# Optimization experiments

Hardware: AMD Instinct MI355X
Metric: run time of the kernel (lower is better)

The kernel has to match this reference:

```python
import jax, jax.numpy as jnp
import numpy as np

LN_EPS = 1e-5  # torch.nn.LayerNorm default


def setup_inputs() -> dict:
    key = jax.random.key(0)
    k1, k2 = jax.random.split(key)
    C = 64
    x = jax.random.normal(k1, (1, C, 64, 96, 96), dtype=jnp.float32)
    ln_gamma = jnp.ones((C,), jnp.float32)
    ln_beta = jnp.zeros((C,), jnp.float32)
    # Conv3d(C, 3C, 1, groups=C) -> per-channel scalar weight [3C] and bias [3C]
    conv_w = jax.random.normal(k2, (3 * C,), dtype=jnp.float32) * 0.02
    conv_b = jnp.zeros((3 * C,), jnp.float32)
    return {"x": x, "ln_gamma": ln_gamma, "ln_beta": ln_beta,
            "conv_w": conv_w, "conv_b": conv_b}


def reference(x, ln_gamma, ln_beta, conv_w, conv_b):
    B, C, D, H, W = x.shape
    N = D * H * W
    xf = x.reshape(B, C, N)  # [B, C, N]

    # LayerNorm over the channel dim (module permutes channels last)
    mean = jnp.mean(xf, axis=1, keepdims=True)
    var = jnp.mean(jnp.square(xf - mean), axis=1, keepdims=True)
    y = (xf - mean) * jax.lax.rsqrt(var + LN_EPS)
    y = y * ln_gamma[None, :, None] + ln_beta[None, :, None]

    # grouped 1x1x1 conv: output channel o reads input channel o // 3
    idx = jnp.arange(3 * C) // 3
    y3 = y[:, idx, :] * conv_w[None, :, None] + conv_b[None, :, None]  # [B, 3C, N]
    q, k, v = jnp.split(y3, 3, axis=1)  # each [B, C, N]

    # channel (cross-covariance) attention: logits [B, C, C]
    logits = jnp.einsum('bcn,bkn->bck', q, k) * (C ** -0.5)
    attn = jax.nn.softmax(logits, axis=-1)  # max-subtraction built in
    out = jnp.einsum('bck,bkn->bcn', attn, v).reshape(B, C, D, H, W)
    return x + out
```

## Files before the change

### kernel.cpp

```cpp
#include <hip/hip_runtime.h>

#define NPOS 589824
#define LN_EPS 1e-5f

typedef _Float16 half8 __attribute__((ext_vector_type(8)));
typedef float f32x4 __attribute__((ext_vector_type(4)));

#define K1_BLOCKS 768
#define CPB 3

__global__ __launch_bounds__(256) void csa_k1(
    const float* __restrict__ x, const float* __restrict__ lng,
    const float* __restrict__ lnb, float* __restrict__ partials,
    float* __restrict__ gfin, int partial_mode)
{
    __shared__ __align__(16) _Float16 Aar[32][264];
    __shared__ __align__(16) _Float16 Bar[32][264];
    const int tid = threadIdx.x;
    const int lane = tid & 63;
    const int wv = tid >> 6;

    #pragma unroll
    for (int r = 22; r < 32; ++r) {
        const _Float16 v = (r == 22) ? (_Float16)1.0f : (_Float16)0.0f;
        for (int ci = tid; ci < 264; ci += 256) { Aar[r][ci] = v; Bar[r][ci] = v; }
    }
    f32x4 acc00 = {0.f,0.f,0.f,0.f}, acc01 = acc00, acc10 = acc00, acc11 = acc00;
    const int row = lane & 15;
    const int kbase = wv * 64 + ((lane >> 4) << 3);
    const int pos0 = blockIdx.x * (CPB * 256);

    for (int ck = 0; ck < CPB; ++ck) {
        const int n = pos0 + ck * 256 + tid;
        float s = 0.f, sq = 0.f;
        float xv[43];
        #pragma unroll
        for (int c = 0; c < 43; ++c) {
            float v = x[c * NPOS + n];
            xv[c] = v; s += v; sq = fmaf(v, v, sq);
        }
        #pragma unroll
        for (int c = 43; c < 64; ++c) {
            float v = x[c * NPOS + n];
            s += v; sq = fmaf(v, v, sq);
        }
        const float mu  = s * (1.f/64.f);
        const float var = fmaf(-mu, mu, sq * (1.f/64.f));
        const float rin = rsqrtf(fmaxf(var, 0.f) + LN_EPS);
        #pragma unroll
        for (int c = 0; c < 43; ++c) {
            float yv = fmaf((xv[c] - mu) * rin, lng[c], lnb[c]);
            _Float16 h = (_Float16)yv;
            if (c < 22)  Aar[c][tid] = h;
            if (c >= 21) Bar[c - 21][tid] = h;
        }
        __syncthreads();
        #pragma unroll
        for (int s2 = 0; s2 < 2; ++s2) {
            const int kk = kbase + s2 * 32;
            half8 a0 = *(const half8*)&Aar[row][kk];
            half8 a1 = *(const half8*)&Aar[row + 16][kk];
            half8 b0 = *(const half8*)&Bar[row][kk];
            half8 b1 = *(const half8*)&Bar[row + 16][kk];
            acc00 = __builtin_amdgcn_mfma_f32_16x16x32_f16(a0, b0, acc00, 0, 0, 0);
            acc01 = __builtin_amdgcn_mfma_f32_16x16x32_f16(a0, b1, acc01, 0, 0, 0);
            acc10 = __builtin_amdgcn_mfma_f32_16x16x32_f16(a1, b0, acc10, 0, 0, 0);
            acc11 = __builtin_amdgcn_mfma_f32_16x16x32_f16(a1, b1, acc11, 0, 0, 0);
        }
        __syncthreads();
    }
    float* G32 = (float*)&Aar[0][0];
    for (int e = tid; e < 1024; e += 256) G32[e] = 0.f;
    __syncthreads();
    const int r0 = (lane >> 4) * 4, c0 = lane & 15;
    #pragma unroll
    for (int r = 0; r < 4; ++r) {
        atomicAdd(&G32[(r0 + r) * 32 + c0],            acc00[r]);
        atomicAdd(&G32[(r0 + r) * 32 + 16 + c0],       acc01[r]);
        atomicAdd(&G32[(16 + r0 + r) * 32 + c0],       acc10[r]);
        atomicAdd(&G32[(16 + r0 + r) * 32 + 16 + c0],  acc11[r]);
    }
    __syncthreads();
    if (partial_mode) {
        for (int e = tid; e < 1024; e += 256) partials[blockIdx.x * 1024 + e] = G32[e];
    } else {
        for (int e = tid; e < 1024; e += 256) atomicAdd(&gfin[e], G32[e]);
    }
}

__global__ __launch_bounds__(256) void csa_k2(const float* __restrict__ partials,
                                              float* __restrict__ gfin)
{
    const int e = blockIdx.x * 256 + threadIdx.x;
    float s = 0.f;
    for (int b = 0; b < K1_BLOCKS; ++b) s += partials[b * 1024 + e];
    gfin[e] = s;
}

__global__ void csa_k3(const float* __restrict__ G, const float* __restrict__ cw,
                       const float* __restrict__ cb, float* __restrict__ M,
                       float* __restrict__ betaO)
{
    const int c = threadIdx.x;
    __shared__ float lg[64][65];
    const float wq = cw[c], bq = cb[c];
    const int a = c / 3;
    const float Sa = G[a * 32 + 22];
    float mx = -1e30f;
    #pragma unroll
    for (int k = 0; k < 64; ++k) {
        const float wk = cw[64 + k], bk = cb[64 + k];
        const int b = (64 + k) / 3 - 21;
        const float Gab = G[a * 32 + b];
        const float Sb  = G[22 * 32 + b];
        float lo = 0.125f * (wq * wk * Gab + wq * bk * Sa + bq * wk * Sb
                             + bq * bk * (float)NPOS);
        lg[c][k] = lo;
        mx = fmaxf(mx, lo);
    }
    float sum = 0.f;
    #pragma unroll
    for (int k = 0; k < 64; ++k) {
        float e = expf(lg[c][k] - mx);
        lg[c][k] = e; sum += e;
    }
    const float inv = 1.f / sum;
    float Ml[22];
    #pragma unroll
    for (int m = 0; m < 22; ++m) Ml[m] = 0.f;
    float bacc = 0.f;
    #pragma unroll
    for (int k = 0; k < 64; ++k) {
        const float attn = lg[c][k] * inv;
        const int mm = (128 + k) / 3 - 42;
        Ml[mm] = fmaf(attn, cw[128 + k], Ml[mm]);
        bacc   = fmaf(attn, cb[128 + k], bacc);
    }
    #pragma unroll
    for (int m = 0; m < 22; ++m) M[c * 22 + m] = Ml[m];
    betaO[c] = bacc;
}

__global__ __launch_bounds__(256) void csa_k4(
    const float* __restrict__ x, const float* __restrict__ lng,
    const float* __restrict__ lnb, const float* __restrict__ M,
    const float* __restrict__ betaO, float* __restrict__ out)
{
    const int n = blockIdx.x * 256 + threadIdx.x;
    float xv[64];
    float s = 0.f, sq = 0.f;
    #pragma unroll
    for (int c = 0; c < 64; ++c) {
        float v = x[c * NPOS + n];
        xv[c] = v; s += v; sq = fmaf(v, v, sq);
    }
    const float mu  = s * (1.f/64.f);
    const float var = fmaf(-mu, mu, sq * (1.f/64.f));
    const float rin = rsqrtf(fmaxf(var, 0.f) + LN_EPS);
    float y[22];
    #pragma unroll
    for (int m = 0; m < 22; ++m)
        y[m] = fmaf((xv[42 + m] - mu) * rin, lng[42 + m], lnb[42 + m]);
    #pragma unroll
    for (int c = 0; c < 64; ++c) {
        float acc = betaO[c];
        #pragma unroll
        for (int m = 0; m < 22; ++m)
            acc = fmaf(M[c * 22 + m], y[m], acc);
        out[c * NPOS + n] = xv[c] + acc;
    }
}

extern "C" void kernel_launch(void* const* d_in, const int* in_sizes, int n_in,
                              void* d_out, int out_size, void* d_ws, size_t ws_size,
                              hipStream_t stream) {
    const float* x   = (const float*)d_in[0];
    const float* lng = (const float*)d_in[1];
    const float* lnb = (const float*)d_in[2];
    const float* cw  = (const float*)d_in[3];
    const float* cb  = (const float*)d_in[4];
    float* out = (float*)d_out;

    float* wsf = (float*)d_ws;
    float* Gf  = wsf;
    float* Mf  = wsf + 1024;
    float* Bf  = wsf + 1024 + 64 * 22;
    float* Pf  = wsf + 4096;

    const size_t need = 16384 + (size_t)K1_BLOCKS * 1024 * 4;
    const int partial = (ws_size >= need) ? 1 : 0;
    if (!partial) hipMemsetAsync(Gf, 0, 1024 * sizeof(float), stream);

    hipLaunchKernelGGL(csa_k1, dim3(K1_BLOCKS), dim3(256), 0, stream,
                       x, lng, lnb, Pf, Gf, partial);
    if (partial)
        hipLaunchKernelGGL(csa_k2, dim3(4), dim3(256), 0, stream, Pf, Gf);
    hipLaunchKernelGGL(csa_k3, dim3(1), dim3(64), 0, stream, Gf, cw, cb, Mf, Bf);
    hipLaunchKernelGGL(csa_k4, dim3(NPOS / 256), dim3(256), 0, stream,
                       x, lng, lnb, Mf, Bf, out);
}
```

Before: 172.3 us.

## Precompute LayerNorm stats in separate pass and reuse in gram and output kernels

Adds a vectorized stats kernel that computes per-position mean and inverse std once and stores them to workspace. The gram kernel then reads only the 43 channels it needs instead of all 64. The output kernel reads stats instead of recomputing them and uses nontemporal stores. This trades an extra full read of x plus a stats buffer for less work and traffic in the gram kernel, and keeps the old path as a fallback when the workspace is small.

Measured after the change: 170.7 us. Within noise of the previous version (-0.9%).

```diff
diff --git a/kernel.cpp b/kernel.cpp
--- a/kernel.cpp
+++ b/kernel.cpp
@@ -5,14 +5,40 @@
 
 typedef _Float16 half8 __attribute__((ext_vector_type(8)));
 typedef float f32x4 __attribute__((ext_vector_type(4)));
+typedef float f32x2 __attribute__((ext_vector_type(2)));
 
 #define K1_BLOCKS 768
 #define CPB 3
 
-__global__ __launch_bounds__(256) void csa_k1(
+
+__global__ __launch_bounds__(256) void csa_stats(
+    const float* __restrict__ x, float* __restrict__ stats )
+{
+    const int g = blockIdx.x * 256 + threadIdx.x;
+    const f32x4* __restrict__ x4 = (const f32x4*)x;
+    f32x4 s = {0.f,0.f,0.f,0.f}, sq = s;
+    #pragma unroll
+    for (int c = 0; c < 64; ++c) {
+        f32x4 v = x4[c * (NPOS/4) + g];
+        s += v;
+        sq += v * v;
+    }
+    f32x4 mu = s * (1.f/64.f);
+    f32x4 var = sq * (1.f/64.f) - mu * mu;
+    f32x4 rin;
+    #pragma unroll
+    for (int j = 0; j < 4; ++j) rin[j] = rsqrtf(fmaxf(var[j], 0.f) + LN_EPS);
+    f32x4* st4 = (f32x4*)stats;
+    f32x4 o0 = {mu[0], rin[0], mu[1], rin[1]};
+    f32x4 o1 = {mu[2], rin[2], mu[3], rin[3]};
+    st4[2*g]     = o0;
+    st4[2*g + 1] = o1;
+}
+
+__global__ __launch_bounds__(256) void csa_gram(
     const float* __restrict__ x, const float* __restrict__ lng,
-    const float* __restrict__ lnb, float* __restrict__ partials,
-    float* __restrict__ gfin, int partial_mode)
+    const float* __restrict__ lnb, const float* __restrict__ stats,
+    float* __restrict__ partials, float* __restrict__ gfin, int partial_mode)
 {
     __shared__ __align__(16) _Float16 Aar[32][264];
     __shared__ __align__(16) _Float16 Bar[32][264];
@@ -29,27 +55,16 @@
     const int row = lane & 15;
     const int kbase = wv * 64 + ((lane >> 4) << 3);
     const int pos0 = blockIdx.x * (CPB * 256);
+    const f32x2* __restrict__ st2 = (const f32x2*)stats;
 
     for (int ck = 0; ck < CPB; ++ck) {
         const int n = pos0 + ck * 256 + tid;
-        float s = 0.f, sq = 0.f;
-        float xv[43];
+        const f32x2 st = st2[n];
+        const float mu = st[0], rin = st[1];
         #pragma unroll
         for (int c = 0; c < 43; ++c) {
             float v = x[c * NPOS + n];
-            xv[c] = v; s += v; sq = fmaf(v, v, sq);
-        }
-        #pragma unroll
-        for (int c = 43; c < 64; ++c) {
-            float v = x[c * NPOS + n];
-            s += v; sq = fmaf(v, v, sq);
-        }
-        const float mu  = s * (1.f/64.f);
-        const float var = fmaf(-mu, mu, sq * (1.f/64.f));
-        const float rin = rsqrtf(fmaxf(var, 0.f) + LN_EPS);
-        #pragma unroll
-        for (int c = 0; c < 43; ++c) {
-            float yv = fmaf((xv[c] - mu) * rin, lng[c], lnb[c]);
+            float yv = fmaf((v - mu) * rin, lng[c], lnb[c]);
             _Float16 h = (_Float16)yv;
             if (c < 22)  Aar[c][tid] = h;
             if (c >= 21) Bar[c - 21][tid] = h;
@@ -143,6 +158,120 @@
 
 __global__ __launch_bounds__(256) void csa_k4(
     const float* __restrict__ x, const float* __restrict__ lng,
+    const float* __restrict__ lnb, const float* __restrict__ stats,
+    const float* __restrict__ M, const float* __restrict__ betaO,
+    float* __restrict__ out)
+{
+    const int n = blockIdx.x * 256 + threadIdx.x;
+    const f32x2 st = ((const f32x2*)stats)[n];
+    const float mu = st[0], rin = st[1];
+    float y[22], xr[22];
+    #pragma unroll
+    for (int m = 0; m < 22; ++m) {
+        float v = x[(42 + m) * NPOS + n];
+        xr[m] = v;
+        y[m] = fmaf((v - mu) * rin, lng[42 + m], lnb[42 + m]);
+    }
+    #pragma unroll
+    for (int c = 0; c < 42; ++c) {
+        float v = x[c * NPOS + n];
+        float acc = betaO[c];
+        #pragma unroll
+        for (int m = 0; m < 22; ++m)
+            acc = fmaf(M[c * 22 + m], y[m], acc);
+        __builtin_nontemporal_store(v + acc, &out[c * NPOS + n]);
+    }
+    #pragma unroll
+    for (int c = 42; c < 64; ++c) {
+        float acc = betaO[c];
+        #pragma unroll
+        for (int m = 0; m < 22; ++m)
+            acc = fmaf(M[c * 22 + m], y[m], acc);
+        __builtin_nontemporal_store(xr[c - 42] + acc, &out[c * NPOS + n]);
+    }
+}
+
+__global__ __launch_bounds__(256) void csa_k1f(
+    const float* __restrict__ x, const float* __restrict__ lng,
+    const float* __restrict__ lnb, float* __restrict__ partials,
+    float* __restrict__ gfin, int partial_mode)
+{
+    __shared__ __align__(16) _Float16 Aar[32][264];
+    __shared__ __align__(16) _Float16 Bar[32][264];
+    const int tid = threadIdx.x;
+    const int lane = tid & 63;
+    const int wv = tid >> 6;
+
+    #pragma unroll
+    for (int r = 22; r < 32; ++r) {
+        const _Float16 v = (r == 22) ? (_Float16)1.0f : (_Float16)0.0f;
+        for (int ci = tid; ci < 264; ci += 256) { Aar[r][ci] = v; Bar[r][ci] = v; }
+    }
+    f32x4 acc00 = {0.f,0.f,0.f,0.f}, acc01 = acc00, acc10 = acc00, acc11 = acc00;
+    const int row = lane & 15;
+    const int kbase = wv * 64 + ((lane >> 4) << 3);
+    const int pos0 = blockIdx.x * (CPB * 256);
+
+    for (int ck = 0; ck < CPB; ++ck) {
+        const int n = pos0 + ck * 256 + tid;
+        float s = 0.f, sq = 0.f;
+        float xv[43];
+        #pragma unroll
+        for (int c = 0; c < 43; ++c) {
+            float v = x[c * NPOS + n];
+            xv[c] = v; s += v; sq = fmaf(v, v, sq);
+        }
+        #pragma unroll
+        for (int c = 43; c < 64; ++c) {
+            float v = x[c * NPOS + n];
+            s += v; sq = fmaf(v, v, sq);
+        }
+        const float mu  = s * (1.f/64.f);
+        const float var = fmaf(-mu, mu, sq * (1.f/64.f));
+        const float rin = rsqrtf(fmaxf(var, 0.f) + LN_EPS);
+        #pragma unroll
+        for (int c = 0; c < 43; ++c) {
+            float yv = fmaf((xv[c] - mu) * rin, lng[c], lnb[c]);
+            _Float16 h = (_Float16)yv;
+            if (c < 22)  Aar[c][tid] = h;
+            if (c >= 21) Bar[c - 21][tid] = h;
+        }
+        __syncthreads();
+        #pragma unroll
+        for (int s2 = 0; s2 < 2; ++s2) {
+            const int kk = kbase + s2 * 32;
+            half8 a0 = *(const half8*)&Aar[row][kk];
+            half8 a1 = *(const half8*)&Aar[row + 16][kk];
+            half8 b0 = *(const half8*)&Bar[row][kk];
+            half8 b1 = *(const half8*)&Bar[row + 16][kk];
+            acc00 = __builtin_amdgcn_mfma_f32_16x16x32_f16(a0, b0, acc00, 0, 0, 0);
+            acc01 = __builtin_amdgcn_mfma_f32_16x16x32_f16(a0, b1, acc01, 0, 0, 0);
+            acc10 = __builtin_amdgcn_mfma_f32_16x16x32_f16(a1, b0, acc10, 0, 0, 0);
+            acc11 = __builtin_amdgcn_mfma_f32_16x16x32_f16(a1, b1, acc11, 0, 0, 0);
+        }
+        __syncthreads();
+    }
+    float* G32 = (float*)&Aar[0][0];
+    for (int e = tid; e < 1024; e += 256) G32[e] = 0.f;
+    __syncthreads();
+    const int r0 = (lane >> 4) * 4, c0 = lane & 15;
+    #pragma unroll
+    for (int r = 0; r < 4; ++r) {
+        atomicAdd(&G32[(r0 + r) * 32 + c0],            acc00[r]);
+        atomicAdd(&G32[(r0 + r) * 32 + 16 + c0],       acc01[r]);
+        atomicAdd(&G32[(16 + r0 + r) * 32 + c0],       acc10[r]);
+        atomicAdd(&G32[(16 + r0 + r) * 32 + 16 + c0],  acc11[r]);
+    }
+    __syncthreads();
+    if (partial_mode) {
+        for (int e = tid; e < 1024; e += 256) partials[blockIdx.x * 1024 + e] = G32[e];
+    } else {
+        for (int e = tid; e < 1024; e += 256) atomicAdd(&gfin[e], G32[e]);
+    }
+}
+
+__global__ __launch_bounds__(256) void csa_k4f(
+    const float* __restrict__ x, const float* __restrict__ lng,
     const float* __restrict__ lnb, const float* __restrict__ M,
     const float* __restrict__ betaO, float* __restrict__ out)
 {
@@ -170,6 +299,7 @@
         out[c * NPOS + n] = xv[c] + acc;
     }
 }
+
 
 extern "C" void kernel_launch(void* const* d_in, const int* in_sizes, int n_in,
                               void* d_out, int out_size, void* d_ws, size_t ws_size,
@@ -185,17 +315,33 @@
     float* Gf  = wsf;
     float* Mf  = wsf + 1024;
     float* Bf  = wsf + 1024 + 64 * 22;
-    float* Pf  = wsf + 4096;
-
-    const size_t need = 16384 + (size_t)K1_BLOCKS * 1024 * 4;
-    const int partial = (ws_size >= need) ? 1 : 0;
-    if (!partial) hipMemsetAsync(Gf, 0, 1024 * sizeof(float), stream);
-
-    hipLaunchKernelGGL(csa_k1, dim3(K1_BLOCKS), dim3(256), 0, stream,
-                       x, lng, lnb, Pf, Gf, partial);
-    if (partial)
+
+    const size_t statsOffB = 16384;
+    const size_t partOffB  = statsOffB + (size_t)NPOS * 8;
+    const size_t needFull  = partOffB + (size_t)K1_BLOCKS * 1024 * 4;
+
+    if (ws_size >= needFull) {
+        float* stats = (float*)((char*)d_ws + statsOffB);
+        float* Pf    = (float*)((char*)d_ws + partOffB);
+        hipLaunchKernelGGL(csa_stats, dim3(NPOS / 1024), dim3(256), 0, stream,
+                           x, stats);
+        hipLaunchKernelGGL(csa_gram, dim3(K1_BLOCKS), dim3(256), 0, stream,
+                           x, lng, lnb, stats, Pf, Gf, 1);
         hipLaunchKernelGGL(csa_k2, dim3(4), dim3(256), 0, stream, Pf, Gf);
-    hipLaunchKernelGGL(csa_k3, dim3(1), dim3(64), 0, stream, Gf, cw, cb, Mf, Bf);
-    hipLaunchKernelGGL(csa_k4, dim3(NPOS / 256), dim3(256), 0, stream,
-                       x, lng, lnb, Mf, Bf, out);
-}
+        hipLaunchKernelGGL(csa_k3, dim3(1), dim3(64), 0, stream, Gf, cw, cb, Mf, Bf);
+        hipLaunchKernelGGL(csa_k4, dim3(NPOS / 256), dim3(256), 0, stream,
+                           x, lng, lnb, stats, Mf, Bf, out);
+    } else {
+        float* Pf = wsf + 4096;
+        const size_t need = 16384 + (size_t)K1_BLOCKS * 1024 * 4;
+        const int partial = (ws_size >= need) ? 1 : 0;
+        if (!partial) hipMemsetAsync(Gf, 0, 1024 * sizeof(float), stream);
+        hipLaunchKernelGGL(csa_k1f, dim3(K1_BLOCKS), dim3(256), 0, stream,
+                           x, lng, lnb, Pf, Gf, partial);
+        if (partial)
+            hipLaunchKernelGGL(csa_k2, dim3(4), dim3(256), 0, stream, Pf, Gf);
+        hipLaunchKernelGGL(csa_k3, dim3(1), dim3(64), 0, stream, Gf, cw, cb, Mf, Bf);
+        hipLaunchKernelGGL(csa_k4f, dim3(NPOS / 256), dim3(256), 0, stream,
+                           x, lng, lnb, Mf, Bf, out);
+    }
+}
```
